# Kernel tuning notes

Hardware: AMD Instinct MI355X
Metric: run time of the kernel (lower is better)

Reference implementation:

```python
import jax, jax.numpy as jnp
import numpy as np

M = 128  # split point: first M units use max-plus, rest use min-plus

def setup_inputs() -> dict:
    key = jax.random.key(0)
    k1, k2 = jax.random.split(key)
    x = jax.random.normal(k1, (2048, 512), dtype=jnp.float32)   # (batch, features_in)
    w = jax.random.normal(k2, (512, 256), dtype=jnp.float32)    # (features_in, units)
    return {"x": x, "w": w}

def reference(x, w):
    # Tropical (max/min-plus) pseudo-matmul.
    # s[b, f, u] = x[b, f] + w[f, u]; reduce over f.
    s_max = x[:, :, None] + w[None, :, :M]          # (batch, f, M)
    s_min = x[:, :, None] + w[None, :, M:]          # (batch, f, units-M)
    hv = jnp.max(s_max, axis=1)                     # (batch, M)
    hw = jnp.min(s_min, axis=1)                     # (batch, units-M)
    return jnp.concatenate([hv, hw], axis=1)        # linear activation = identity
```

## Files before the change

kernel.cpp:

```cpp
#include <hip/hip_runtime.h>
#include <math.h>


#define FEAT  512
#define UNITS 256
#define BR    8
#define KW    64
#define NW    8
#define NQ    (KW / 4)

__device__ __forceinline__ float max3(float a, float b, float c) {
    return fmaxf(fmaxf(a, b), c);
}

__device__ __forceinline__ void load_xquad(const float* __restrict__ lds, int kb, int q,
                                           float4* __restrict__ xb) {
    #pragma unroll
    for (int r = 0; r < BR; ++r)
        xb[r] = *(const float4*)&lds[r * FEAT + kb + q * 4];
}

__device__ __forceinline__ void load_wquad(const float* __restrict__ wp, int q,
                                           float4* __restrict__ wb) {
    #pragma unroll
    for (int k = 0; k < 4; ++k)
        wb[k] = *(const float4*)(wp + (size_t)(q * 4 + k) * UNITS);
}

__device__ __forceinline__ void compute_quad(const float4* __restrict__ xb,
                                             const float4* __restrict__ wq,
                                             float sgn, float4* __restrict__ acc) {
    const float4 w0 = make_float4(wq[0].x*sgn, wq[0].y*sgn, wq[0].z*sgn, wq[0].w*sgn);
    const float4 w1 = make_float4(wq[1].x*sgn, wq[1].y*sgn, wq[1].z*sgn, wq[1].w*sgn);
    const float4 w2 = make_float4(wq[2].x*sgn, wq[2].y*sgn, wq[2].z*sgn, wq[2].w*sgn);
    const float4 w3 = make_float4(wq[3].x*sgn, wq[3].y*sgn, wq[3].z*sgn, wq[3].w*sgn);
    #pragma unroll
    for (int r = 0; r < BR; ++r) {
        const float4 a = xb[r];
        float4 A = acc[r];
        A.x = max3(A.x, fmaf(a.x, sgn, w0.x), fmaf(a.y, sgn, w1.x));
        A.x = max3(A.x, fmaf(a.z, sgn, w2.x), fmaf(a.w, sgn, w3.x));
        A.y = max3(A.y, fmaf(a.x, sgn, w0.y), fmaf(a.y, sgn, w1.y));
        A.y = max3(A.y, fmaf(a.z, sgn, w2.y), fmaf(a.w, sgn, w3.y));
        A.z = max3(A.z, fmaf(a.x, sgn, w0.z), fmaf(a.y, sgn, w1.z));
        A.z = max3(A.z, fmaf(a.z, sgn, w2.z), fmaf(a.w, sgn, w3.z));
        A.w = max3(A.w, fmaf(a.x, sgn, w0.w), fmaf(a.y, sgn, w1.w));
        A.w = max3(A.w, fmaf(a.z, sgn, w2.w), fmaf(a.w, sgn, w3.w));
        acc[r] = A;
    }
}

__global__ __launch_bounds__(512) void tropical_kernel(const float* __restrict__ x,
                                                       const float* __restrict__ w,
                                                       float* __restrict__ out) {
    __shared__ float lds[NW * BR * UNITS];
    const int tid  = threadIdx.x;
    const int lane = tid & 63;
    const int wv   = __builtin_amdgcn_readfirstlane(tid >> 6);
    const int u0   = lane * 4;
    const float sgn = (lane < 32) ? 1.0f : -1.0f;
    const int row0 = blockIdx.x * BR;
    const int kb   = wv * KW;

    {
        const float4* src = (const float4*)(x + (size_t)row0 * FEAT);
        ((float4*)lds)[tid]       = src[tid];
        ((float4*)lds)[tid + 512] = src[tid + 512];
    }

    const float* wp = w + (size_t)kb * UNITS + u0;

    float4 acc[BR];
    #pragma unroll
    for (int r = 0; r < BR; ++r)
        acc[r] = make_float4(-__builtin_inff(), -__builtin_inff(),
                             -__builtin_inff(), -__builtin_inff());

    float4 xA[BR], xB[BR], wA[4], wB[4];
    load_wquad(wp, 0, wA);

    __syncthreads();
    load_xquad(lds, kb, 0, xA);

    #pragma unroll 1
    for (int q = 0; q < NQ; q += 2) {
        load_wquad(wp, q + 1, wB);
        load_xquad(lds, kb, q + 1, xB);
        compute_quad(xA, wA, sgn, acc);
        if (q + 2 < NQ) {
            load_wquad(wp, q + 2, wA);
            load_xquad(lds, kb, q + 2, xA);
        }
        compute_quad(xB, wB, sgn, acc);
    }

    __syncthreads();
    #pragma unroll
    for (int r = 0; r < BR; ++r)
        *(float4*)&lds[((wv * BR + r) * UNITS) + u0] = acc[r];
    __syncthreads();

    const int r  = tid >> 6;
    const int uo = (tid & 63) * 4;
    float4 v = *(const float4*)&lds[(0 * BR + r) * UNITS + uo];
    #pragma unroll
    for (int j = 1; j < NW; ++j) {
        const float4 p = *(const float4*)&lds[(j * BR + r) * UNITS + uo];
        v.x = fmaxf(v.x, p.x);
        v.y = fmaxf(v.y, p.y);
        v.z = fmaxf(v.z, p.z);
        v.w = fmaxf(v.w, p.w);
    }
    const float so = (uo < 128) ? 1.0f : -1.0f;
    *(float4*)&out[(size_t)(row0 + r) * UNITS + uo] =
        make_float4(v.x * so, v.y * so, v.z * so, v.w * so);
}

extern "C" void kernel_launch(void* const* d_in, const int* in_sizes, int n_in,
                              void* d_out, int out_size, void* d_ws, size_t ws_size,
                              hipStream_t stream) {
    const float* x = (const float*)d_in[0];
    const float* w = (const float*)d_in[1];
    float* out = (float*)d_out;

    tropical_kernel<<<dim3(2048 / BR), dim3(512), 0, stream>>>(x, w, out);
}
```

Measured before the change: 68.34 us.

## Give each lane eight units and split the feature range across wave halves

Each lane now covers 8 output units instead of 4, and the two 32-lane halves of a wave each reduce a different 32-feature slice. The halves are combined with v_permlane32_swap before the LDS cross-wave reduction. The goal is more reuse of each x value loaded from LDS (fewer ds_reads per max op) and half the LDS stores at the end. In exchange the accumulator and W buffers grow to 16+16 float4 registers, and launch_bounds(512,2) may force register spills.

```diff
diff --git a/kernel.cpp b/kernel.cpp
--- a/kernel.cpp
+++ b/kernel.cpp
@@ -7,60 +7,74 @@
 #define BR    8
 #define KW    64
 #define NW    8
-#define NQ    (KW / 4)
+#define NS    8
 
 __device__ __forceinline__ float max3(float a, float b, float c) {
     return fmaxf(fmaxf(a, b), c);
 }
 
-__device__ __forceinline__ void load_xquad(const float* __restrict__ lds, int kb, int q,
+__device__ __forceinline__ void load_xstep(const float* __restrict__ lds, int xbase, int s,
                                            float4* __restrict__ xb) {
     #pragma unroll
     for (int r = 0; r < BR; ++r)
-        xb[r] = *(const float4*)&lds[r * FEAT + kb + q * 4];
+        xb[r] = *(const float4*)&lds[r * FEAT + xbase + s * 4];
 }
 
-__device__ __forceinline__ void load_wquad(const float* __restrict__ wp, int q,
+__device__ __forceinline__ void load_wstep(const float* __restrict__ wp, int s,
                                            float4* __restrict__ wb) {
     #pragma unroll
-    for (int k = 0; k < 4; ++k)
-        wb[k] = *(const float4*)(wp + (size_t)(q * 4 + k) * UNITS);
-}
-
-__device__ __forceinline__ void compute_quad(const float4* __restrict__ xb,
-                                             const float4* __restrict__ wq,
-                                             float sgn, float4* __restrict__ acc) {
-    const float4 w0 = make_float4(wq[0].x*sgn, wq[0].y*sgn, wq[0].z*sgn, wq[0].w*sgn);
-    const float4 w1 = make_float4(wq[1].x*sgn, wq[1].y*sgn, wq[1].z*sgn, wq[1].w*sgn);
-    const float4 w2 = make_float4(wq[2].x*sgn, wq[2].y*sgn, wq[2].z*sgn, wq[2].w*sgn);
-    const float4 w3 = make_float4(wq[3].x*sgn, wq[3].y*sgn, wq[3].z*sgn, wq[3].w*sgn);
-    #pragma unroll
-    for (int r = 0; r < BR; ++r) {
-        const float4 a = xb[r];
-        float4 A = acc[r];
-        A.x = max3(A.x, fmaf(a.x, sgn, w0.x), fmaf(a.y, sgn, w1.x));
-        A.x = max3(A.x, fmaf(a.z, sgn, w2.x), fmaf(a.w, sgn, w3.x));
-        A.y = max3(A.y, fmaf(a.x, sgn, w0.y), fmaf(a.y, sgn, w1.y));
-        A.y = max3(A.y, fmaf(a.z, sgn, w2.y), fmaf(a.w, sgn, w3.y));
-        A.z = max3(A.z, fmaf(a.x, sgn, w0.z), fmaf(a.y, sgn, w1.z));
-        A.z = max3(A.z, fmaf(a.z, sgn, w2.z), fmaf(a.w, sgn, w3.z));
-        A.w = max3(A.w, fmaf(a.x, sgn, w0.w), fmaf(a.y, sgn, w1.w));
-        A.w = max3(A.w, fmaf(a.z, sgn, w2.w), fmaf(a.w, sgn, w3.w));
-        acc[r] = A;
+    for (int k = 0; k < 4; ++k) {
+        wb[2 * k]     = *(const float4*)(wp + (size_t)(s * 4 + k) * UNITS);
+        wb[2 * k + 1] = *(const float4*)(wp + (size_t)(s * 4 + k) * UNITS + 4);
     }
 }
 
-__global__ __launch_bounds__(512) void tropical_kernel(const float* __restrict__ x,
-                                                       const float* __restrict__ w,
-                                                       float* __restrict__ out) {
+__device__ __forceinline__ void compute_step(const float4* __restrict__ xb,
+                                             const float4* __restrict__ wq,
+                                             float sgn, float4* __restrict__ acc) {
+    #pragma unroll
+    for (int r = 0; r < BR; ++r) {
+        const float4 a  = xb[r];
+        const float4 af = make_float4(a.x * sgn, a.y * sgn, a.z * sgn, a.w * sgn);
+        #pragma unroll
+        for (int g = 0; g < 2; ++g) {
+            const float4 w0 = wq[0 + g];
+            const float4 w1 = wq[2 + g];
+            const float4 w2 = wq[4 + g];
+            const float4 w3 = wq[6 + g];
+            float4 A = acc[r * 2 + g];
+            A.x = max3(A.x, fmaf(w0.x, sgn, af.x), fmaf(w1.x, sgn, af.y));
+            A.x = max3(A.x, fmaf(w2.x, sgn, af.z), fmaf(w3.x, sgn, af.w));
+            A.y = max3(A.y, fmaf(w0.y, sgn, af.x), fmaf(w1.y, sgn, af.y));
+            A.y = max3(A.y, fmaf(w2.y, sgn, af.z), fmaf(w3.y, sgn, af.w));
+            A.z = max3(A.z, fmaf(w0.z, sgn, af.x), fmaf(w1.z, sgn, af.y));
+            A.z = max3(A.z, fmaf(w2.z, sgn, af.z), fmaf(w3.z, sgn, af.w));
+            A.w = max3(A.w, fmaf(w0.w, sgn, af.x), fmaf(w1.w, sgn, af.y));
+            A.w = max3(A.w, fmaf(w2.w, sgn, af.z), fmaf(w3.w, sgn, af.w));
+            acc[r * 2 + g] = A;
+        }
+    }
+}
+
+__device__ __forceinline__ float half_swap_max(float v) {
+    float a = v, b = v;
+    asm("v_permlane32_swap_b32 %0, %1" : "+v"(a), "+v"(b));
+    return fmaxf(a, b);
+}
+
+__global__ __launch_bounds__(512, 2) void tropical_kernel(const float* __restrict__ x,
+                                                          const float* __restrict__ w,
+                                                          float* __restrict__ out) {
     __shared__ float lds[NW * BR * UNITS];
     const int tid  = threadIdx.x;
     const int lane = tid & 63;
     const int wv   = __builtin_amdgcn_readfirstlane(tid >> 6);
-    const int u0   = lane * 4;
-    const float sgn = (lane < 32) ? 1.0f : -1.0f;
+    const int h    = lane >> 5;
+    const int u0   = (lane & 31) * 8;
+    const float sgn = ((lane & 31) < 16) ? 1.0f : -1.0f;
     const int row0 = blockIdx.x * BR;
     const int kb   = wv * KW;
+    const int xbase = kb + h * 32;
 
     {
         const float4* src = (const float4*)(x + (size_t)row0 * FEAT);
@@ -68,36 +82,48 @@
         ((float4*)lds)[tid + 512] = src[tid + 512];
     }
 
-    const float* wp = w + (size_t)kb * UNITS + u0;
+    const float* wp = w + (size_t)xbase * UNITS + u0;
 
-    float4 acc[BR];
+    float4 acc[BR * 2];
     #pragma unroll
-    for (int r = 0; r < BR; ++r)
-        acc[r] = make_float4(-__builtin_inff(), -__builtin_inff(),
+    for (int i = 0; i < BR * 2; ++i)
+        acc[i] = make_float4(-__builtin_inff(), -__builtin_inff(),
                              -__builtin_inff(), -__builtin_inff());
 
-    float4 xA[BR], xB[BR], wA[4], wB[4];
-    load_wquad(wp, 0, wA);
+    float4 xA[BR], xB[BR], wA[8], wB[8];
+    load_wstep(wp, 0, wA);
 
     __syncthreads();
-    load_xquad(lds, kb, 0, xA);
+    load_xstep(lds, xbase, 0, xA);
 
     #pragma unroll 1
-    for (int q = 0; q < NQ; q += 2) {
-        load_wquad(wp, q + 1, wB);
-        load_xquad(lds, kb, q + 1, xB);
-        compute_quad(xA, wA, sgn, acc);
-        if (q + 2 < NQ) {
-            load_wquad(wp, q + 2, wA);
-            load_xquad(lds, kb, q + 2, xA);
+    for (int s = 0; s < NS; s += 2) {
+        load_wstep(wp, s + 1, wB);
+        load_xstep(lds, xbase, s + 1, xB);
+        compute_step(xA, wA, sgn, acc);
+        if (s + 2 < NS) {
+            load_wstep(wp, s + 2, wA);
+            load_xstep(lds, xbase, s + 2, xA);
         }
-        compute_quad(xB, wB, sgn, acc);
+        compute_step(xB, wB, sgn, acc);
+    }
+
+    #pragma unroll
+    for (int i = 0; i < BR * 2; ++i) {
+        acc[i].x = half_swap_max(acc[i].x);
+        acc[i].y = half_swap_max(acc[i].y);
+        acc[i].z = half_swap_max(acc[i].z);
+        acc[i].w = half_swap_max(acc[i].w);
     }
 
     __syncthreads();
-    #pragma unroll
-    for (int r = 0; r < BR; ++r)
-        *(float4*)&lds[((wv * BR + r) * UNITS) + u0] = acc[r];
+    if (lane < 32) {
+        #pragma unroll
+        for (int r = 0; r < BR; ++r) {
+            *(float4*)&lds[(wv * BR + r) * UNITS + u0]     = acc[r * 2];
+            *(float4*)&lds[(wv * BR + r) * UNITS + u0 + 4] = acc[r * 2 + 1];
+        }
+    }
     __syncthreads();
 
     const int r  = tid >> 6;
```

New measurement: 72.51 us. 1.06x slower.

## Split waves by max/min half and feature quarter, drop sign-trick FMAs and LDS x staging

Applied to the files above, without the earlier changes.

Waves are now assigned one half of the units (max-plus or min-plus) and a quarter of the feature dimension. Each wave handles two units per lane over 128 features, using plain adds with templated max or min instead of sign-multiplied FMAs. x is read directly from global memory rather than staged through LDS, and the cross-wave reduction now combines only four partials per half. Waves per EU are pinned to 2. The intent is to remove the per-element sign multiply and the LDS staging barrier. In exchange, x is read from global or cache redundantly across waves, and the weight loads are narrower float2 accesses.

```diff
diff --git a/kernel.cpp b/kernel.cpp
--- a/kernel.cpp
+++ b/kernel.cpp
@@ -5,115 +5,128 @@
 #define FEAT  512
 #define UNITS 256
 #define BR    8
-#define KW    64
 #define NW    8
-#define NQ    (KW / 4)
+#define KW    128
+#define NS    (KW / 4)
+#define LDSZ  24576
 
-__device__ __forceinline__ float max3(float a, float b, float c) {
+__device__ __forceinline__ float max3f(float a, float b, float c) {
     return fmaxf(fmaxf(a, b), c);
 }
+__device__ __forceinline__ float min3f(float a, float b, float c) {
+    return fminf(fminf(a, b), c);
+}
 
-__device__ __forceinline__ void load_xquad(const float* __restrict__ lds, int kb, int q,
+__device__ __forceinline__ void load_xstep(const float* __restrict__ xp, int s,
                                            float4* __restrict__ xb) {
     #pragma unroll
     for (int r = 0; r < BR; ++r)
-        xb[r] = *(const float4*)&lds[r * FEAT + kb + q * 4];
+        xb[r] = *(const float4*)(xp + r * FEAT + s * 4);
 }
 
-__device__ __forceinline__ void load_wquad(const float* __restrict__ wp, int q,
-                                           float4* __restrict__ wb) {
+__device__ __forceinline__ void load_wstep(const float* __restrict__ wp, int s,
+                                           float2* __restrict__ wb) {
     #pragma unroll
-    for (int k = 0; k < 4; ++k)
-        wb[k] = *(const float4*)(wp + (size_t)(q * 4 + k) * UNITS);
+    for (int j = 0; j < 4; ++j)
+        wb[j] = *(const float2*)(wp + (size_t)(s * 4 + j) * UNITS);
 }
 
-__device__ __forceinline__ void compute_quad(const float4* __restrict__ xb,
-                                             const float4* __restrict__ wq,
-                                             float sgn, float4* __restrict__ acc) {
-    const float4 w0 = make_float4(wq[0].x*sgn, wq[0].y*sgn, wq[0].z*sgn, wq[0].w*sgn);
-    const float4 w1 = make_float4(wq[1].x*sgn, wq[1].y*sgn, wq[1].z*sgn, wq[1].w*sgn);
-    const float4 w2 = make_float4(wq[2].x*sgn, wq[2].y*sgn, wq[2].z*sgn, wq[2].w*sgn);
-    const float4 w3 = make_float4(wq[3].x*sgn, wq[3].y*sgn, wq[3].z*sgn, wq[3].w*sgn);
+template<bool ISMAX>
+__device__ __forceinline__ void compute_step(const float4* __restrict__ xb,
+                                             const float2* __restrict__ wq,
+                                             float2* __restrict__ acc) {
     #pragma unroll
     for (int r = 0; r < BR; ++r) {
         const float4 a = xb[r];
-        float4 A = acc[r];
-        A.x = max3(A.x, fmaf(a.x, sgn, w0.x), fmaf(a.y, sgn, w1.x));
-        A.x = max3(A.x, fmaf(a.z, sgn, w2.x), fmaf(a.w, sgn, w3.x));
-        A.y = max3(A.y, fmaf(a.x, sgn, w0.y), fmaf(a.y, sgn, w1.y));
-        A.y = max3(A.y, fmaf(a.z, sgn, w2.y), fmaf(a.w, sgn, w3.y));
-        A.z = max3(A.z, fmaf(a.x, sgn, w0.z), fmaf(a.y, sgn, w1.z));
-        A.z = max3(A.z, fmaf(a.z, sgn, w2.z), fmaf(a.w, sgn, w3.z));
-        A.w = max3(A.w, fmaf(a.x, sgn, w0.w), fmaf(a.y, sgn, w1.w));
-        A.w = max3(A.w, fmaf(a.z, sgn, w2.w), fmaf(a.w, sgn, w3.w));
+        const float t0x = a.x + wq[0].x, t0y = a.x + wq[0].y;
+        const float t1x = a.y + wq[1].x, t1y = a.y + wq[1].y;
+        const float t2x = a.z + wq[2].x, t2y = a.z + wq[2].y;
+        const float t3x = a.w + wq[3].x, t3y = a.w + wq[3].y;
+        float2 A = acc[r];
+        if (ISMAX) {
+            A.x = max3f(A.x, t0x, t1x);  A.x = max3f(A.x, t2x, t3x);
+            A.y = max3f(A.y, t0y, t1y);  A.y = max3f(A.y, t2y, t3y);
+        } else {
+            A.x = min3f(A.x, t0x, t1x);  A.x = min3f(A.x, t2x, t3x);
+            A.y = min3f(A.y, t0y, t1y);  A.y = min3f(A.y, t2y, t3y);
+        }
         acc[r] = A;
     }
 }
 
-__global__ __launch_bounds__(512) void tropical_kernel(const float* __restrict__ x,
-                                                       const float* __restrict__ w,
-                                                       float* __restrict__ out) {
-    __shared__ float lds[NW * BR * UNITS];
+template<bool ISMAX>
+__device__ __forceinline__ void main_loop(const float* __restrict__ xp,
+                                          const float* __restrict__ wp,
+                                          float2* __restrict__ acc) {
+    float4 xA[BR], xB[BR];
+    float2 wA[4], wB[4];
+    load_xstep(xp, 0, xA);
+    load_wstep(wp, 0, wA);
+    #pragma unroll 1
+    for (int s = 0; s < NS; s += 2) {
+        load_xstep(xp, s + 1, xB);
+        load_wstep(wp, s + 1, wB);
+        compute_step<ISMAX>(xA, wA, acc);
+        if (s + 2 < NS) {
+            load_xstep(xp, s + 2, xA);
+            load_wstep(wp, s + 2, wA);
+        }
+        compute_step<ISMAX>(xB, wB, acc);
+    }
+}
+
+__global__ __launch_bounds__(512)
+__attribute__((amdgpu_waves_per_eu(2, 2)))
+void tropical_kernel(const float* __restrict__ x,
+                     const float* __restrict__ w,
+                     float* __restrict__ out) {
+    __shared__ float lds[LDSZ];
     const int tid  = threadIdx.x;
     const int lane = tid & 63;
     const int wv   = __builtin_amdgcn_readfirstlane(tid >> 6);
-    const int u0   = lane * 4;
-    const float sgn = (lane < 32) ? 1.0f : -1.0f;
+    const int ks   = (wv & 3) * KW;
+    const int half = wv >> 2;
+    const int u0   = lane * 2;
     const int row0 = blockIdx.x * BR;
-    const int kb   = wv * KW;
 
-    {
-        const float4* src = (const float4*)(x + (size_t)row0 * FEAT);
-        ((float4*)lds)[tid]       = src[tid];
-        ((float4*)lds)[tid + 512] = src[tid + 512];
-    }
+    const float* xp = x + (size_t)row0 * FEAT + ks;
+    const float* wp = w + (size_t)ks * UNITS + half * 128 + u0;
 
-    const float* wp = w + (size_t)kb * UNITS + u0;
-
-    float4 acc[BR];
+    float2 acc[BR];
+    const float init = half ? __builtin_inff() : -__builtin_inff();
     #pragma unroll
     for (int r = 0; r < BR; ++r)
-        acc[r] = make_float4(-__builtin_inff(), -__builtin_inff(),
-                             -__builtin_inff(), -__builtin_inff());
+        acc[r] = make_float2(init, init);
 
-    float4 xA[BR], xB[BR], wA[4], wB[4];
-    load_wquad(wp, 0, wA);
+    if (half == 0) main_loop<true >(xp, wp, acc);
+    else           main_loop<false>(xp, wp, acc);
 
-    __syncthreads();
-    load_xquad(lds, kb, 0, xA);
-
-    #pragma unroll 1
-    for (int q = 0; q < NQ; q += 2) {
-        load_wquad(wp, q + 1, wB);
-        load_xquad(lds, kb, q + 1, xB);
-        compute_quad(xA, wA, sgn, acc);
-        if (q + 2 < NQ) {
-            load_wquad(wp, q + 2, wA);
-            load_xquad(lds, kb, q + 2, xA);
-        }
-        compute_quad(xB, wB, sgn, acc);
-    }
-
-    __syncthreads();
     #pragma unroll
     for (int r = 0; r < BR; ++r)
-        *(float4*)&lds[((wv * BR + r) * UNITS) + u0] = acc[r];
+        *(float2*)&lds[(wv * BR + r) * 128 + u0] = acc[r];
     __syncthreads();
 
     const int r  = tid >> 6;
-    const int uo = (tid & 63) * 4;
-    float4 v = *(const float4*)&lds[(0 * BR + r) * UNITS + uo];
-    #pragma unroll
-    for (int j = 1; j < NW; ++j) {
-        const float4 p = *(const float4*)&lds[(j * BR + r) * UNITS + uo];
-        v.x = fmaxf(v.x, p.x);
-        v.y = fmaxf(v.y, p.y);
-        v.z = fmaxf(v.z, p.z);
-        v.w = fmaxf(v.w, p.w);
+    const int u4 = (tid & 63) * 4;
+    const int hh = u4 >> 7;
+    const int uo = u4 & 127;
+    const float4 p0 = *(const float4*)&lds[((hh * 4 + 0) * BR + r) * 128 + uo];
+    const float4 p1 = *(const float4*)&lds[((hh * 4 + 1) * BR + r) * 128 + uo];
+    const float4 p2 = *(const float4*)&lds[((hh * 4 + 2) * BR + r) * 128 + uo];
+    const float4 p3 = *(const float4*)&lds[((hh * 4 + 3) * BR + r) * 128 + uo];
+    float4 v;
+    if (hh == 0) {
+        v.x = fmaxf(fmaxf(p0.x, p1.x), fmaxf(p2.x, p3.x));
+        v.y = fmaxf(fmaxf(p0.y, p1.y), fmaxf(p2.y, p3.y));
+        v.z = fmaxf(fmaxf(p0.z, p1.z), fmaxf(p2.z, p3.z));
+        v.w = fmaxf(fmaxf(p0.w, p1.w), fmaxf(p2.w, p3.w));
+    } else {
+        v.x = fminf(fminf(p0.x, p1.x), fminf(p2.x, p3.x));
+        v.y = fminf(fminf(p0.y, p1.y), fminf(p2.y, p3.y));
+        v.z = fminf(fminf(p0.z, p1.z), fminf(p2.z, p3.z));
+        v.w = fminf(fminf(p0.w, p1.w), fminf(p2.w, p3.w));
     }
-    const float so = (uo < 128) ? 1.0f : -1.0f;
-    *(float4*)&out[(size_t)(row0 + r) * UNITS + uo] =
-        make_float4(v.x * so, v.y * so, v.z * so, v.w * so);
+    *(float4*)&out[(size_t)(row0 + r) * UNITS + u4] = v;
 }
 
 extern "C" void kernel_launch(void* const* d_in, const int* in_sizes, int n_in,
```

Measured after the change: 71.45 us. +4.6%, slower.
